# Performance work log

Measured on AMD Instinct MI355X. Metric: run time of the kernel, lower is better.

Reference implementation:

```python
import jax, jax.numpy as jnp
import numpy as np
from jax import lax

# --- block geometry (matches init_kwargs) ---
B = 8
DIM = 192
HEADS = 6
KEY_DIM = DIM // HEADS  # 32, attn_ratio=1 so d == key_dim and dh == DIM
HX, WX = 32, 32         # search region
HZ, WZ = 16, 16         # template region
T = 1                   # template_number
L = HX * WX + T * HZ * WZ  # 1280 tokens
MLP_HIDDEN = int(DIM * 4.0)
BN_EPS = 1e-5


def _build_bias_idx():
    """Replicates Attention.__init__ global_att=True bias-index construction.
    Unique-offset ids may be permuted vs torch dict-insertion order, which is an
    equivalent reparameterization of the (randomly initialized) bias table."""
    g = np.stack(np.meshgrid(np.arange(HX), np.arange(WX), indexing='ij'), -1).reshape(-1, 2)
    pts = [g]
    for i in range(T):
        r = np.arange(HX + HZ * i, WX + WZ * (i + 1))
        g2 = np.stack(np.meshgrid(r, r, indexing='ij'), -1).reshape(-1, 2)
        pts.append(g2)
    p = np.concatenate(pts, 0)                      # (L, 2)
    off = np.abs(p[:, None, :] - p[None, :, :])     # (L, L, 2)
    key = off[:, :, 0].astype(np.int64) * 4096 + off[:, :, 1]
    uniq, inv = np.unique(key, return_inverse=True)
    return inv.reshape(L, L).astype(np.int32), int(len(uniq))


def setup_inputs() -> dict:
    key = jax.random.key(0)
    ks = jax.random.split(key, 16)
    idx_np, n_off = _build_bias_idx()
    s = 0.02
    return {
        'xz': jax.random.normal(ks[0], (B, L, DIM), jnp.float32),
        'bias_idx': jnp.asarray(idx_np),
        'ln1_g': jnp.ones((DIM,), jnp.float32),
        'ln1_b': jnp.zeros((DIM,), jnp.float32),
        'wqkv': jax.random.normal(ks[1], (DIM, 3 * DIM), jnp.float32) * s,
        'bqkv': jnp.zeros((3 * DIM,), jnp.float32),
        'wproj': jax.random.normal(ks[2], (DIM, DIM), jnp.float32) * s,
        'bproj': jnp.zeros((DIM,), jnp.float32),
        'bias_table': jax.random.normal(ks[3], (HEADS, n_off), jnp.float32) * 0.1,
        'conv_w': jax.random.normal(ks[4], (3, 3, 1, DIM), jnp.float32) * 0.1,  # depthwise HWIO
        'bn_scale': jnp.ones((DIM,), jnp.float32) + jax.random.normal(ks[5], (DIM,), jnp.float32) * 0.01,
        'bn_bias': jax.random.normal(ks[6], (DIM,), jnp.float32) * 0.01,
        'ln2_g': jnp.ones((DIM,), jnp.float32),
        'ln2_b': jnp.zeros((DIM,), jnp.float32),
        'w1': jax.random.normal(ks[7], (DIM, MLP_HIDDEN), jnp.float32) * s,
        'b1': jnp.zeros((MLP_HIDDEN,), jnp.float32),
        'w2': jax.random.normal(ks[8], (MLP_HIDDEN, DIM), jnp.float32) * s,
        'b2': jnp.zeros((DIM,), jnp.float32),
    }


def _layernorm(x, g, b, eps=1e-5):
    mu = jnp.mean(x, -1, keepdims=True)
    var = jnp.mean(jnp.square(x - mu), -1, keepdims=True)
    return (x - mu) * lax.rsqrt(var + eps) * g + b


def reference(xz, bias_idx, ln1_g, ln1_b, wqkv, bqkv, wproj, bproj, bias_table,
              conv_w, bn_scale, bn_bias, ln2_g, ln2_b, w1, b1, w2, b2):
    Bn, N, D = xz.shape
    scale = KEY_DIM ** -0.5
    # --- Attention (LeViT-style with gathered relative-position bias) ---
    h = _layernorm(xz, ln1_g, ln1_b)
    qkv = (h @ wqkv + bqkv).reshape(Bn, N, HEADS, 3 * KEY_DIM)
    q, k, v = jnp.split(qkv, 3, axis=3)            # each (B, N, H, key_dim)
    bias = bias_table[:, bias_idx]                  # (H, N, N) gather
    attn = jnp.einsum('bnhd,bmhd->bhnm', q, k) * scale + bias
    attn = jax.nn.softmax(attn, axis=-1)
    o = jnp.einsum('bhnm,bmhd->bnhd', attn, v).reshape(Bn, N, D)
    xm = xz + o @ wproj + bproj
    # --- depthwise local conv (Conv2d_BN, BN folded to scale/bias) per segment ---
    segs = []
    start = 0
    for (Hh, Ww) in [(HX, WX)] + [(HZ, WZ)] * T:
        xc = xm[:, start:start + Hh * Ww, :].reshape(Bn, Hh, Ww, D)
        xc = lax.conv_general_dilated(
            xc, conv_w, window_strides=(1, 1), padding='SAME',
            dimension_numbers=('NHWC', 'HWIO', 'NHWC'), feature_group_count=D)
        xc = xc * bn_scale + bn_bias
        segs.append(xc.reshape(Bn, Hh * Ww, D))
        start += Hh * Ww
    xm = jnp.concatenate(segs, axis=1)
    # --- MLP with pre-LN (exact GELU, matching nn.GELU default) ---
    m = _layernorm(xm, ln2_g, ln2_b)
    m = jax.nn.gelu(m @ w1 + b1, approximate=False) @ w2 + b2
    return xm + m
```

## Files before the change

kernel.cpp:

```cpp
#include <hip/hip_runtime.h>
#include <hip/hip_bf16.h>

#define BATCH 8
#define LTOK 1280
#define DIMC 192
#define HEADS 6
#define KD 32
#define HID 768
#define NROWS (BATCH*LTOK)

typedef short s16x8 __attribute__((ext_vector_type(8)));
typedef float f32x4 __attribute__((ext_vector_type(4)));
typedef unsigned short u16;

#define QS (0.17677669529663687f * 1.4426950408889634f)
#define L2E 1.4426950408889634f

__device__ __forceinline__ u16 f2bf(float x) {
    unsigned u = __float_as_uint(x);
    u = (u + 0x7FFFu + ((u >> 16) & 1u)) >> 16;
    return (u16)u;
}
__device__ __forceinline__ float bf2f(u16 v) { return __uint_as_float((unsigned)v << 16); }
__device__ __forceinline__ float bflo(unsigned u) { return __uint_as_float(u << 16); }
__device__ __forceinline__ float bfhi(unsigned u) { return __uint_as_float(u & 0xffff0000u); }
__device__ __forceinline__ float fexp2(float x) { float r; asm("v_exp_f32 %0, %1" : "=v"(r) : "v"(x)); return r; }
__device__ __forceinline__ float frcp(float x)  { float r; asm("v_rcp_f32 %0, %1" : "=v"(r) : "v"(x)); return r; }

__global__ __launch_bounds__(256) void pre_a(const float* __restrict__ w0,
                                             u16* __restrict__ o0,
                                             const float* __restrict__ xz,
                                             const float* __restrict__ ln1g,
                                             const float* __restrict__ ln1b,
                                             u16* __restrict__ hbuf) {
    __shared__ float s[16][17];
    int f = blockIdx.x;
    if (f >= 432) {
        int row = (f - 432) * 4 + (threadIdx.x >> 6);
        int lane = threadIdx.x & 63;
        const float* xr = xz + (size_t)row * DIMC;
        float v0 = xr[lane], v1 = xr[lane + 64], v2 = xr[lane + 128];
        float sm = v0 + v1 + v2;
        float ss = v0 * v0 + v1 * v1 + v2 * v2;
        #pragma unroll
        for (int off = 32; off; off >>= 1) {
            sm += __shfl_xor(sm, off);
            ss += __shfl_xor(ss, off);
        }
        float mu  = sm * (1.0f / DIMC);
        float var = ss * (1.0f / DIMC) - mu * mu;
        float inv = rsqrtf(var + 1e-5f);
        u16* yr = hbuf + (size_t)row * DIMC;
        yr[lane]       = f2bf((v0 - mu) * inv * ln1g[lane]       + ln1b[lane]);
        yr[lane + 64]  = f2bf((v1 - mu) * inv * ln1g[lane + 64]  + ln1b[lane + 64]);
        yr[lane + 128] = f2bf((v2 - mu) * inv * ln1g[lane + 128] + ln1b[lane + 128]);
        return;
    }
    int tn = f % 36, tk = f / 36;
    int tx = threadIdx.x & 15, ty = threadIdx.x >> 4;
    s[ty][tx] = w0[(size_t)(tk * 16 + ty) * 576 + tn * 16 + tx];
    __syncthreads();
    o0[(size_t)(tn * 16 + ty) * 192 + tk * 16 + tx] = f2bf(s[tx][ty]);
}

__global__ __launch_bounds__(256) void qkv_mega(const u16* __restrict__ A,
                                                const u16* __restrict__ Wt,
                                                const float* __restrict__ bias,
                                                u16* __restrict__ qb,
                                                u16* __restrict__ kp,
                                                u16* __restrict__ vp,
                                                const int* __restrict__ bidx,
                                                const float* __restrict__ btab,
                                                int n_off, u16* __restrict__ bmp,
                                                const float* __restrict__ wp,
                                                const float* __restrict__ wf1,
                                                const float* __restrict__ wf2,
                                                u16* __restrict__ op,
                                                u16* __restrict__ of1,
                                                u16* __restrict__ of2) {
    int bid = blockIdx.x;
    if (bid >= 9960) {
        __shared__ float s[16][17];
        int f2 = bid - 9960;
        const float* in; u16* out; int K, N, tn, tk;
        if (f2 < 144)      { in = wp;  out = op;  K = 192; N = 192; tn = f2 % 12; tk = f2 / 12; }
        else if (f2 < 720) { in = wf1; out = of1; K = 192; N = 768; int q = f2 - 144; tn = q % 48; tk = q / 48; }
        else               { in = wf2; out = of2; K = 768; N = 192; int q = f2 - 720; tn = q % 12; tk = q / 12; }
        int tx = threadIdx.x & 15, ty = threadIdx.x >> 4;
        s[ty][tx] = in[(size_t)(tk * 16 + ty) * N + tn * 16 + tx];
        __syncthreads();
        out[(size_t)(tn * 16 + ty) * K + tk * 16 + tx] = f2bf(s[tx][ty]);
        return;
    }
    if (bid >= 360) {
        int fb = bid - 360;
        int qt = fb / 120;
        int rem = fb - qt * 120;
        int T = rem / 6, h = rem - (rem / 6) * 6;
        int tid = threadIdx.x;
        int half = tid >> 7, L = (tid >> 1) & 63, j4 = (tid & 1) * 4;
        int n = qt * 16 + (L & 15);
        int m = T * 64 + half * 32 + ((L >> 4) << 3) + j4;
        int4 iv = *(const int4*)(bidx + (size_t)n * LTOK + m);
        const float* tab = btab + (size_t)h * n_off;
        ushort4 o;
        o.x = f2bf(tab[iv.x] * L2E);
        o.y = f2bf(tab[iv.y] * L2E);
        o.z = f2bf(tab[iv.z] * L2E);
        o.w = f2bf(tab[iv.w] * L2E);
        *(ushort4*)(bmp + (size_t)(h * 80 + qt) * 20480 + T * 1024 + tid * 4) = o;
        return;
    }
    int bx = bid % 9, by = bid / 9;
    int tid = threadIdx.x;
    int L = tid & 63, w = tid >> 6;
    int r = L & 15, g = L >> 4;
    int m0 = by * 256 + w * 64;
    int n0 = bx * 64;

    f32x4 acc[4][4] = {};
    const u16* Ab = A + (size_t)(m0 + r) * 192 + g * 8;
    const u16* Wb = Wt + (size_t)(n0 + r) * 192 + g * 8;
    #pragma unroll 6
    for (int k0 = 0; k0 < 192; k0 += 32) {
        s16x8 af[4];
        #pragma unroll
        for (int mi = 0; mi < 4; ++mi)
            af[mi] = *(const s16x8*)(Ab + (size_t)mi * 16 * 192 + k0);
        #pragma unroll
        for (int nn = 0; nn < 4; ++nn) {
            s16x8 bf = *(const s16x8*)(Wb + (size_t)nn * 16 * 192 + k0);
            #pragma unroll
            for (int mi = 0; mi < 4; ++mi)
                acc[mi][nn] = __builtin_amdgcn_mfma_f32_16x16x32_bf16(af[mi], bf, acc[mi][nn], 0, 0, 0);
        }
    }
    #pragma unroll
    for (int mi = 0; mi < 4; ++mi)
    #pragma unroll
    for (int nn = 0; nn < 4; ++nn) {
        int cb = n0 + nn * 16;
        int h  = cb / 96, c0 = cb % 96;
        int reg = c0 >> 5;
        #pragma unroll
        for (int i = 0; i < 4; ++i) {
            int row = m0 + mi * 16 + g * 4 + i;
            float v = acc[mi][nn][i] + bias[cb + r];
            if (reg == 0) {
                v *= QS;
                qb[(size_t)row * DIMC + h * 32 + (c0 & 31) + r] = f2bf(v);
            } else {
                int b_ = row / LTOK, t = row - b_ * LTOK;
                int T = t >> 5, it = t & 31;
                int d = (c0 & 31) + r;
                if (reg == 1) {
                    int which = (it >> 2) & 1;
                    int ik = ((it >> 3) << 2) | (it & 3);
                    int Lk = ((d >> 3) << 4) + ik;
                    kp[((size_t)(b_ * HEADS + h) * 40 + T) * 1024 + which * 512 + Lk * 8 + (d & 7)] = f2bf(v);
                } else {
                    int Lv = ((it >> 3) << 4) + (d & 15);
                    vp[((size_t)(b_ * HEADS + h) * 40 + T) * 1024 + (d >> 4) * 512 + Lv * 8 + (it & 7)] = f2bf(v);
                }
            }
        }
    }
}

__global__ __launch_bounds__(256) void attn_mfma(const u16* __restrict__ qb,
                                                 const u16* __restrict__ kp,
                                                 const u16* __restrict__ vp,
                                                 const u16* __restrict__ bmp,
                                                 u16* __restrict__ ob) {
    __shared__ __align__(16) u16 kvs[2][2][2048];
    int tid = threadIdx.x;
    int L = tid & 63, w = tid >> 6;
    int r = L & 15, g = L >> 4;
    int L8 = L * 8;

    int bid = blockIdx.x;
    int work = (bid & 7) * 120 + (bid >> 3);
    int b  = work & 7;
    int hq = work >> 3;
    int qt = (hq % 20) * 4 + w;
    int h  = hq / 20;

    s16x8 qf = *(const s16x8*)(qb + (size_t)(b * LTOK + qt * 16 + r) * DIMC + h * 32 + g * 8);

    int skv = w >> 1, half = w & 1;
    const u16* gs = (skv ? vp : kp) + (size_t)(b * HEADS + h) * 40 * 1024 + L8;
    u16* dst0 = &kvs[0][skv][half * 1024 + L8];
    u16* dst1 = &kvs[1][skv][half * 1024 + L8];

    const u16* bmr = bmp + (size_t)(h * 80 + qt) * 20480 + L8;

    f32x4 acc0 = {0.f, 0.f, 0.f, 0.f}, acc1 = {0.f, 0.f, 0.f, 0.f};
    float lsum = 0.f;

    {
        int4 pA = *(const int4*)(gs + half * 1024);
        int4 pB = *(const int4*)(gs + half * 1024 + 512);
        *(int4*)dst0 = pA;
        *(int4*)(dst0 + 512) = pB;
    }
    int4 cb0 = *(const int4*)(bmr);
    int4 cb1 = *(const int4*)(bmr + 512);
    __syncthreads();

    f32x4 s0, s1, s2, s3;
    {
        const u16* kb = &kvs[0][0][0];
        f32x4 z0, z1, z2, z3;
        z0[0] = bflo(cb0.x); z0[1] = bfhi(cb0.x); z0[2] = bflo(cb0.y); z0[3] = bfhi(cb0.y);
        z1[0] = bflo(cb0.z); z1[1] = bfhi(cb0.z); z1[2] = bflo(cb0.w); z1[3] = bfhi(cb0.w);
        z2[0] = bflo(cb1.x); z2[1] = bfhi(cb1.x); z2[2] = bflo(cb1.y); z2[3] = bfhi(cb1.y);
        z3[0] = bflo(cb1.z); z3[1] = bfhi(cb1.z); z3[2] = bflo(cb1.w); z3[3] = bfhi(cb1.w);
        s16x8 kf0 = *(const s16x8*)(kb + L8);
        s16x8 kf1 = *(const s16x8*)(kb + 512 + L8);
        s16x8 kf2 = *(const s16x8*)(kb + 1024 + L8);
        s16x8 kf3 = *(const s16x8*)(kb + 1536 + L8);
        s0 = __builtin_amdgcn_mfma_f32_16x16x32_bf16(kf0, qf, z0, 0, 0, 0);
        s1 = __builtin_amdgcn_mfma_f32_16x16x32_bf16(kf1, qf, z1, 0, 0, 0);
        s2 = __builtin_amdgcn_mfma_f32_16x16x32_bf16(kf2, qf, z2, 0, 0, 0);
        s3 = __builtin_amdgcn_mfma_f32_16x16x32_bf16(kf3, qf, z3, 0, 0, 0);
    }

    #pragma unroll 1
    for (int T = 0; T < 20; ++T) {
        int4 nA, nB, nb0, nb1;
        if (T < 19) {
            nA  = *(const int4*)(gs + (size_t)(2 * T + 2 + half) * 1024);
            nB  = *(const int4*)(gs + (size_t)(2 * T + 2 + half) * 1024 + 512);
            nb0 = *(const int4*)(bmr + (size_t)(T + 1) * 1024);
            nb1 = *(const int4*)(bmr + (size_t)(T + 1) * 1024 + 512);
        }
        __builtin_amdgcn_s_setprio(1);
        float p[16];
        #pragma unroll
        for (int j = 0; j < 4; ++j) {
            p[j]      = fexp2(s0[j]);
            p[4 + j]  = fexp2(s1[j]);
            p[8 + j]  = fexp2(s2[j]);
            p[12 + j] = fexp2(s3[j]);
        }
        float t0 = ((p[0] + p[1]) + (p[2] + p[3])) + ((p[4] + p[5]) + (p[6] + p[7]));
        float t1 = ((p[8] + p[9]) + (p[10] + p[11])) + ((p[12] + p[13]) + (p[14] + p[15]));
        lsum += t0 + t1;
        union { unsigned u[4]; s16x8 v; } pa, pb;
        #pragma unroll
        for (int j = 0; j < 4; ++j) {
            asm("v_cvt_pk_bf16_f32 %0, %1, %2" : "=v"(pa.u[j]) : "v"(p[2 * j]), "v"(p[2 * j + 1]));
            asm("v_cvt_pk_bf16_f32 %0, %1, %2" : "=v"(pb.u[j]) : "v"(p[8 + 2 * j]), "v"(p[9 + 2 * j]));
        }
        const u16* vb = &kvs[T & 1][1][0];
        s16x8 v0 = *(const s16x8*)(vb + L8);
        s16x8 v1 = *(const s16x8*)(vb + 512 + L8);
        s16x8 v2 = *(const s16x8*)(vb + 1024 + L8);
        s16x8 v3 = *(const s16x8*)(vb + 1536 + L8);
        acc0 = __builtin_amdgcn_mfma_f32_16x16x32_bf16(pa.v, v0, acc0, 0, 0, 0);
        acc1 = __builtin_amdgcn_mfma_f32_16x16x32_bf16(pa.v, v1, acc1, 0, 0, 0);
        acc0 = __builtin_amdgcn_mfma_f32_16x16x32_bf16(pb.v, v2, acc0, 0, 0, 0);
        acc1 = __builtin_amdgcn_mfma_f32_16x16x32_bf16(pb.v, v3, acc1, 0, 0, 0);
        __builtin_amdgcn_s_setprio(0);

        if (T < 19) {
            u16* d = (T & 1) ? dst0 : dst1;
            *(int4*)d = nA;
            *(int4*)(d + 512) = nB;
        }
        __syncthreads();
        if (T < 19) {
            const u16* kb = &kvs[(T + 1) & 1][0][0];
            f32x4 z0, z1, z2, z3;
            z0[0] = bflo(nb0.x); z0[1] = bfhi(nb0.x); z0[2] = bflo(nb0.y); z0[3] = bfhi(nb0.y);
            z1[0] = bflo(nb0.z); z1[1] = bfhi(nb0.z); z1[2] = bflo(nb0.w); z1[3] = bfhi(nb0.w);
            z2[0] = bflo(nb1.x); z2[1] = bfhi(nb1.x); z2[2] = bflo(nb1.y); z2[3] = bfhi(nb1.y);
            z3[0] = bflo(nb1.z); z3[1] = bfhi(nb1.z); z3[2] = bflo(nb1.w); z3[3] = bfhi(nb1.w);
            s16x8 kf0 = *(const s16x8*)(kb + L8);
            s16x8 kf1 = *(const s16x8*)(kb + 512 + L8);
            s16x8 kf2 = *(const s16x8*)(kb + 1024 + L8);
            s16x8 kf3 = *(const s16x8*)(kb + 1536 + L8);
            __builtin_amdgcn_s_setprio(1);
            s0 = __builtin_amdgcn_mfma_f32_16x16x32_bf16(kf0, qf, z0, 0, 0, 0);
            s1 = __builtin_amdgcn_mfma_f32_16x16x32_bf16(kf1, qf, z1, 0, 0, 0);
            s2 = __builtin_amdgcn_mfma_f32_16x16x32_bf16(kf2, qf, z2, 0, 0, 0);
            s3 = __builtin_amdgcn_mfma_f32_16x16x32_bf16(kf3, qf, z3, 0, 0, 0);
            __builtin_amdgcn_s_setprio(0);
        }
    }

    float lr = lsum;
    lr += __shfl_xor(lr, 16);
    lr += __shfl_xor(lr, 32);
    #pragma unroll
    for (int i = 0; i < 4; ++i) {
        float linv = frcp(__shfl(lr, 4 * g + i));
        size_t orow = (size_t)(b * LTOK + qt * 16 + 4 * g + i) * DIMC + h * 32 + r;
        ob[orow]      = f2bf(acc0[i] * linv);
        ob[orow + 16] = f2bf(acc1[i] * linv);
    }
}

template<int ACT, int RES, int OBF, int K, int MTILE>
__global__ __launch_bounds__(256) void gemm_mfma(const u16* __restrict__ A,
                                                 const u16* __restrict__ Wt,
                                                 const float* __restrict__ bias,
                                                 const float* __restrict__ R,
                                                 void* __restrict__ Cp,
                                                 int N) {
    constexpr int SUB = MTILE / 64;
    int tid = threadIdx.x;
    int L = tid & 63, w = tid >> 6;
    int r = L & 15, g = L >> 4;
    int m0 = blockIdx.y * MTILE + w * (16 * SUB);
    int n0 = blockIdx.x * 64;

    f32x4 acc[SUB][4] = {};
    const u16* Ab = A + (size_t)(m0 + r) * K + g * 8;
    const u16* Wb = Wt + (size_t)(n0 + r) * K + g * 8;
    #pragma unroll 6
    for (int k0 = 0; k0 < K; k0 += 32) {
        s16x8 af[SUB];
        #pragma unroll
        for (int mi = 0; mi < SUB; ++mi)
            af[mi] = *(const s16x8*)(Ab + (size_t)mi * 16 * K + k0);
        #pragma unroll
        for (int nn = 0; nn < 4; ++nn) {
            s16x8 bf = *(const s16x8*)(Wb + (size_t)nn * 16 * K + k0);
            #pragma unroll
            for (int mi = 0; mi < SUB; ++mi)
                acc[mi][nn] = __builtin_amdgcn_mfma_f32_16x16x32_bf16(af[mi], bf, acc[mi][nn], 0, 0, 0);
        }
    }

    #pragma unroll
    for (int mi = 0; mi < SUB; ++mi)
    #pragma unroll
    for (int nn = 0; nn < 4; ++nn) {
        int cb = n0 + nn * 16;
        #pragma unroll
        for (int i = 0; i < 4; ++i) {
            int row = m0 + mi * 16 + g * 4 + i;
            float v = acc[mi][nn][i] + bias[cb + r];
            if (ACT == 1) {
                float u = v;
                float y = 0.7978845608028654f * (u + 0.044715f * u * u * u);
                float e2 = fexp2(y * 2.885390081777927f);
                v = u - u * frcp(e2 + 1.0f);
            }
            if (RES) v += R[(size_t)row * N + cb + r];
            if (OBF) ((u16*)Cp)[(size_t)row * N + cb + r] = f2bf(v);
            else     ((float*)Cp)[(size_t)row * N + cb + r] = v;
        }
    }
}

__global__ __launch_bounds__(256) void conv_ln_kernel(const u16* __restrict__ xm,
                                                      const float* __restrict__ w,
                                                      const float* __restrict__ scale,
                                                      const float* __restrict__ bias,
                                                      const float* __restrict__ g2,
                                                      const float* __restrict__ b2,
                                                      float* __restrict__ xm2,
                                                      u16* __restrict__ y) {
    int row = blockIdx.x * 4 + (threadIdx.x >> 6);
    int lane = threadIdx.x & 63;
    int b = row / LTOK, t = row - b * LTOK;
    int H, W, base, y0, x0;
    if (t < 1024) { H = 32; W = 32; base = 0;    y0 = t >> 5;            x0 = t & 31; }
    else          { H = 16; W = 16; base = 1024; int tt = t - 1024; y0 = tt >> 4; x0 = tt & 15; }
    float a0 = 0.f, a1 = 0.f, a2 = 0.f;
    #pragma unroll
    for (int ky = 0; ky < 3; ++ky) {
        int yy = y0 + ky - 1;
        if (yy < 0 || yy >= H) continue;
        #pragma unroll
        for (int kx = 0; kx < 3; ++kx) {
            int xx = x0 + kx - 1;
            if (xx < 0 || xx >= W) continue;
            const u16* xr = xm + (size_t)(b * LTOK + base + yy * W + xx) * DIMC;
            const float* wr = w + (ky * 3 + kx) * DIMC;
            a0 += wr[lane]       * bf2f(xr[lane]);
            a1 += wr[lane + 64]  * bf2f(xr[lane + 64]);
            a2 += wr[lane + 128] * bf2f(xr[lane + 128]);
        }
    }
    float v0 = a0 * scale[lane]       + bias[lane];
    float v1 = a1 * scale[lane + 64]  + bias[lane + 64];
    float v2 = a2 * scale[lane + 128] + bias[lane + 128];
    float* xr2 = xm2 + (size_t)row * DIMC;
    xr2[lane] = v0; xr2[lane + 64] = v1; xr2[lane + 128] = v2;
    float s = v0 + v1 + v2;
    float ss = v0 * v0 + v1 * v1 + v2 * v2;
    #pragma unroll
    for (int off = 32; off; off >>= 1) {
        s  += __shfl_xor(s, off);
        ss += __shfl_xor(ss, off);
    }
    float mu  = s * (1.0f / DIMC);
    float var = ss * (1.0f / DIMC) - mu * mu;
    float inv = rsqrtf(var + 1e-5f);
    u16* yr = y + (size_t)row * DIMC;
    yr[lane]       = f2bf((v0 - mu) * inv * g2[lane]       + b2[lane]);
    yr[lane + 64]  = f2bf((v1 - mu) * inv * g2[lane + 64]  + b2[lane + 64]);
    yr[lane + 128] = f2bf((v2 - mu) * inv * g2[lane + 128] + b2[lane + 128]);
}

extern "C" void kernel_launch(void* const* d_in, const int* in_sizes, int n_in,
                              void* d_out, int out_size, void* d_ws, size_t ws_size,
                              hipStream_t stream) {
    const float* xz       = (const float*)d_in[0];
    const int*   bidx     = (const int*)  d_in[1];
    const float* ln1_g    = (const float*)d_in[2];
    const float* ln1_b    = (const float*)d_in[3];
    const float* wqkv     = (const float*)d_in[4];
    const float* bqkv     = (const float*)d_in[5];
    const float* wproj    = (const float*)d_in[6];
    const float* bproj    = (const float*)d_in[7];
    const float* btab     = (const float*)d_in[8];
    const float* conv_w   = (const float*)d_in[9];
    const float* bn_scale = (const float*)d_in[10];
    const float* bn_bias  = (const float*)d_in[11];
    const float* ln2_g    = (const float*)d_in[12];
    const float* ln2_b    = (const float*)d_in[13];
    const float* w1       = (const float*)d_in[14];
    const float* b1       = (const float*)d_in[15];
    const float* w2       = (const float*)d_in[16];
    const float* b2       = (const float*)d_in[17];
    int n_off = in_sizes[8] / HEADS;
    float* out = (float*)d_out;

    char* wsb = (char*)d_ws;
    u16*  hbuf   = (u16*)(wsb + 0);
    u16*  ob     = (u16*)(wsb + 0);
    u16*  wqkvT  = (u16*)(wsb + 3932160);
    u16*  wprojT = (u16*)(wsb + 4153344);
    u16*  w1T    = (u16*)(wsb + 4227072);
    u16*  w2T    = (u16*)(wsb + 4521984);
    u16*  bmp    = (u16*)(wsb + 4816896);
    u16*  hid    = (u16*)(wsb + 4816896);
    u16*  kp     = (u16*)(wsb + 24477696);
    u16*  vp     = (u16*)(wsb + 28409856);
    float* xm2   = (float*)(wsb + 24477696);
    u16*  qb     = (u16*)(wsb + 32342016);
    u16*  xm     = (u16*)(wsb + 32342016);

    pre_a<<<432 + NROWS / 4, 256, 0, stream>>>(wqkv, wqkvT, xz, ln1_g, ln1_b, hbuf);
    qkv_mega<<<11256, 256, 0, stream>>>(
        hbuf, wqkvT, bqkv, qb, kp, vp,
        bidx, btab, n_off, bmp,
        wproj, w1, w2, wprojT, w1T, w2T);
    attn_mfma<<<960, 256, 0, stream>>>(qb, kp, vp, bmp, ob);
    gemm_mfma<0,1,1,DIMC,128><<<dim3(DIMC / 64, NROWS / 128), 256, 0, stream>>>(
        ob, wprojT, bproj, xz, xm, DIMC);
    conv_ln_kernel<<<NROWS / 4, 256, 0, stream>>>(
        xm, conv_w, bn_scale, bn_bias, ln2_g, ln2_b, xm2, hbuf);
    gemm_mfma<1,0,1,DIMC,256><<<dim3(HID / 64, NROWS / 256), 256, 0, stream>>>(
        hbuf, w1T, b1, nullptr, hid, HID);
    gemm_mfma<0,1,0,HID,128><<<dim3(DIMC / 64, NROWS / 128), 256, 0, stream>>>(
        hid, w2T, b2, xm2, out, DIMC);
}
```

Measured before the change: 120.5 us.

## Split attention KV loop across two wave groups with LDS reduction

The attention kernel doubles its block to 512 threads. Two groups of four waves each take half of the key/value tiles for the same query tiles, which halves the serial loop length per wave. The partial outputs and softmax sums are then combined through shared memory before normalisation. This adds parallelism to hide the latency of the dependent loop, at the cost of a reduction step, an extra barrier and more LDS per block, which may lower the number of resident blocks.

```diff
diff --git a/kernel.cpp b/kernel.cpp
--- a/kernel.cpp
+++ b/kernel.cpp
@@ -167,39 +167,41 @@
     }
 }
 
-__global__ __launch_bounds__(256) void attn_mfma(const u16* __restrict__ qb,
+__global__ __launch_bounds__(512) void attn_mfma(const u16* __restrict__ qb,
                                                  const u16* __restrict__ kp,
                                                  const u16* __restrict__ vp,
                                                  const u16* __restrict__ bmp,
                                                  u16* __restrict__ ob) {
-    __shared__ __align__(16) u16 kvs[2][2][2048];
+    __shared__ __align__(16) u16 kvs[2][2][2][2048];
     int tid = threadIdx.x;
     int L = tid & 63, w = tid >> 6;
     int r = L & 15, g = L >> 4;
     int L8 = L * 8;
+    int qw = w & 3, kh = w >> 2;
 
     int bid = blockIdx.x;
     int work = (bid & 7) * 120 + (bid >> 3);
     int b  = work & 7;
     int hq = work >> 3;
-    int qt = (hq % 20) * 4 + w;
+    int qt = (hq % 20) * 4 + qw;
     int h  = hq / 20;
 
     s16x8 qf = *(const s16x8*)(qb + (size_t)(b * LTOK + qt * 16 + r) * DIMC + h * 32 + g * 8);
 
-    int skv = w >> 1, half = w & 1;
-    const u16* gs = (skv ? vp : kp) + (size_t)(b * HEADS + h) * 40 * 1024 + L8;
-    u16* dst0 = &kvs[0][skv][half * 1024 + L8];
-    u16* dst1 = &kvs[1][skv][half * 1024 + L8];
-
-    const u16* bmr = bmp + (size_t)(h * 80 + qt) * 20480 + L8;
+    int shalf = w >> 2, skv = (w >> 1) & 1, stile = w & 1;
+    const u16* gs = (skv ? vp : kp) + (size_t)(b * HEADS + h) * 40 * 1024
+                    + (size_t)(shalf * 20 + stile) * 1024 + L8;
+    u16* dst0 = &kvs[0][shalf][skv][stile * 1024 + L8];
+    u16* dst1 = &kvs[1][shalf][skv][stile * 1024 + L8];
+
+    const u16* bmr = bmp + (size_t)(h * 80 + qt) * 20480 + (size_t)kh * 10 * 1024 + L8;
 
     f32x4 acc0 = {0.f, 0.f, 0.f, 0.f}, acc1 = {0.f, 0.f, 0.f, 0.f};
     float lsum = 0.f;
 
     {
-        int4 pA = *(const int4*)(gs + half * 1024);
-        int4 pB = *(const int4*)(gs + half * 1024 + 512);
+        int4 pA = *(const int4*)(gs);
+        int4 pB = *(const int4*)(gs + 512);
         *(int4*)dst0 = pA;
         *(int4*)(dst0 + 512) = pB;
     }
@@ -209,7 +211,7 @@
 
     f32x4 s0, s1, s2, s3;
     {
-        const u16* kb = &kvs[0][0][0];
+        const u16* kb = &kvs[0][kh][0][0];
         f32x4 z0, z1, z2, z3;
         z0[0] = bflo(cb0.x); z0[1] = bfhi(cb0.x); z0[2] = bflo(cb0.y); z0[3] = bfhi(cb0.y);
         z1[0] = bflo(cb0.z); z1[1] = bfhi(cb0.z); z1[2] = bflo(cb0.w); z1[3] = bfhi(cb0.w);
@@ -226,11 +228,11 @@
     }
 
     #pragma unroll 1
-    for (int T = 0; T < 20; ++T) {
+    for (int T = 0; T < 10; ++T) {
         int4 nA, nB, nb0, nb1;
-        if (T < 19) {
-            nA  = *(const int4*)(gs + (size_t)(2 * T + 2 + half) * 1024);
-            nB  = *(const int4*)(gs + (size_t)(2 * T + 2 + half) * 1024 + 512);
+        if (T < 9) {
+            nA  = *(const int4*)(gs + (size_t)(2 * T + 2) * 1024);
+            nB  = *(const int4*)(gs + (size_t)(2 * T + 2) * 1024 + 512);
             nb0 = *(const int4*)(bmr + (size_t)(T + 1) * 1024);
             nb1 = *(const int4*)(bmr + (size_t)(T + 1) * 1024 + 512);
         }
@@ -252,7 +254,7 @@
             asm("v_cvt_pk_bf16_f32 %0, %1, %2" : "=v"(pa.u[j]) : "v"(p[2 * j]), "v"(p[2 * j + 1]));
             asm("v_cvt_pk_bf16_f32 %0, %1, %2" : "=v"(pb.u[j]) : "v"(p[8 + 2 * j]), "v"(p[9 + 2 * j]));
         }
-        const u16* vb = &kvs[T & 1][1][0];
+        const u16* vb = &kvs[T & 1][kh][1][0];
         s16x8 v0 = *(const s16x8*)(vb + L8);
         s16x8 v1 = *(const s16x8*)(vb + 512 + L8);
         s16x8 v2 = *(const s16x8*)(vb + 1024 + L8);
@@ -263,14 +265,14 @@
         acc1 = __builtin_amdgcn_mfma_f32_16x16x32_bf16(pb.v, v3, acc1, 0, 0, 0);
         __builtin_amdgcn_s_setprio(0);
 
-        if (T < 19) {
+        if (T < 9) {
             u16* d = (T & 1) ? dst0 : dst1;
             *(int4*)d = nA;
             *(int4*)(d + 512) = nB;
         }
         __syncthreads();
-        if (T < 19) {
-            const u16* kb = &kvs[(T + 1) & 1][0][0];
+        if (T < 9) {
+            const u16* kb = &kvs[(T + 1) & 1][kh][0][0];
             f32x4 z0, z1, z2, z3;
             z0[0] = bflo(nb0.x); z0[1] = bfhi(nb0.x); z0[2] = bflo(nb0.y); z0[3] = bfhi(nb0.y);
             z1[0] = bflo(nb0.z); z1[1] = bfhi(nb0.z); z1[2] = bflo(nb0.w); z1[3] = bfhi(nb0.w);
@@ -289,15 +291,28 @@
         }
     }
 
-    float lr = lsum;
-    lr += __shfl_xor(lr, 16);
-    lr += __shfl_xor(lr, 32);
-    #pragma unroll
-    for (int i = 0; i < 4; ++i) {
-        float linv = frcp(__shfl(lr, 4 * g + i));
-        size_t orow = (size_t)(b * LTOK + qt * 16 + 4 * g + i) * DIMC + h * 32 + r;
-        ob[orow]      = f2bf(acc0[i] * linv);
-        ob[orow + 16] = f2bf(acc1[i] * linv);
+    float* red = (float*)&kvs[0][0][0][0];
+    if (kh == 1) {
+        float* rd = red + (size_t)(qw * 64 + L) * 9;
+        rd[0] = acc0[0]; rd[1] = acc0[1]; rd[2] = acc0[2]; rd[3] = acc0[3];
+        rd[4] = acc1[0]; rd[5] = acc1[1]; rd[6] = acc1[2]; rd[7] = acc1[3];
+        rd[8] = lsum;
+    }
+    __syncthreads();
+    if (kh == 0) {
+        const float* rd = red + (size_t)(qw * 64 + L) * 9;
+        acc0[0] += rd[0]; acc0[1] += rd[1]; acc0[2] += rd[2]; acc0[3] += rd[3];
+        acc1[0] += rd[4]; acc1[1] += rd[5]; acc1[2] += rd[6]; acc1[3] += rd[7];
+        float lr = lsum + rd[8];
+        lr += __shfl_xor(lr, 16);
+        lr += __shfl_xor(lr, 32);
+        #pragma unroll
+        for (int i = 0; i < 4; ++i) {
+            float linv = frcp(__shfl(lr, 4 * g + i));
+            size_t orow = (size_t)(b * LTOK + qt * 16 + 4 * g + i) * DIMC + h * 32 + r;
+            ob[orow]      = f2bf(acc0[i] * linv);
+            ob[orow + 16] = f2bf(acc1[i] * linv);
+        }
     }
 }
 
@@ -450,7 +465,7 @@
         hbuf, wqkvT, bqkv, qb, kp, vp,
         bidx, btab, n_off, bmp,
         wproj, w1, w2, wprojT, w1T, w2T);
-    attn_mfma<<<960, 256, 0, stream>>>(qb, kp, vp, bmp, ob);
+    attn_mfma<<<960, 512, 0, stream>>>(qb, kp, vp, bmp, ob);
     gemm_mfma<0,1,1,DIMC,128><<<dim3(DIMC / 64, NROWS / 128), 256, 0, stream>>>(
         ob, wprojT, bproj, xz, xm, DIMC);
     conv_ln_kernel<<<NROWS / 4, 256, 0, stream>>>(
```

New measurement: 122.6 us. No clear change (+1.7%).
